# Optimization experiments

Measured on AMD Instinct MI355X. Metric: run time of the kernel, lower is better.

Reference implementation:

```python
import jax, jax.numpy as jnp
import numpy as np

NUM_ORDERS = 100
NUM_MACHINES = 40
NUM_AGVS = 64
EMBED = 128


def setup_inputs() -> dict:
    key = jax.random.key(0)
    ks = jax.random.split(key, 12)
    s = 0.05
    h_order = jax.random.normal(ks[0], (NUM_ORDERS, EMBED), jnp.float32)
    h_agv = jax.random.normal(ks[1], (NUM_AGVS, EMBED), jnp.float32)
    h_waiting = jax.random.normal(ks[2], (NUM_MACHINES, EMBED), jnp.float32)
    h_buffer = jax.random.normal(ks[3], (NUM_MACHINES, EMBED), jnp.float32)
    W1d = jax.random.normal(ks[4], (3 * EMBED, EMBED), jnp.float32) * s
    b1d = jnp.zeros((EMBED,), jnp.float32)
    W2d = jax.random.normal(ks[5], (EMBED,), jnp.float32) * s
    b2d = jnp.zeros((1,), jnp.float32)
    W1p = jax.random.normal(ks[6], (2 * EMBED, EMBED), jnp.float32) * s
    b1p = jnp.zeros((EMBED,), jnp.float32)
    W2p = jax.random.normal(ks[7], (EMBED,), jnp.float32) * s
    b2p = jnp.zeros((1,), jnp.float32)
    n_logits = NUM_AGVS * (NUM_ORDERS * NUM_MACHINES + NUM_MACHINES)
    action_mask = jax.random.randint(ks[8], (n_logits,), 0, 2).astype(jnp.int32)
    return dict(h_order=h_order, h_agv=h_agv, h_waiting=h_waiting, h_buffer=h_buffer,
                W1d=W1d, b1d=b1d, W2d=W2d, b2d=b2d,
                W1p=W1p, b1p=b1p, W2p=W2p, b2p=b2p,
                action_mask=action_mask)


def reference(h_order, h_agv, h_waiting, h_buffer,
              W1d, b1d, W2d, b2d, W1p, b1p, W2p, b2p, action_mask):
    O, M, A, D = NUM_ORDERS, NUM_MACHINES, NUM_AGVS, EMBED
    # dispatch pairs: order_idx = repeat_interleave(arange(O), M); machine_idx = tile(arange(M), O)
    order_idx = jnp.repeat(jnp.arange(O), M)            # [O*M]
    machine_idx = jnp.tile(jnp.arange(M), O)            # [O*M]
    pair = jnp.concatenate([h_order[order_idx], h_waiting[machine_idx]], axis=1)  # [O*M, 2D]
    agv_b = jnp.broadcast_to(h_agv[:, None, :], (A, O * M, D))                    # [A, O*M, D]
    disp_in = jnp.concatenate([agv_b, jnp.broadcast_to(pair[None], (A, O * M, 2 * D))], axis=-1)  # [A, O*M, 3D]
    hdd = jax.nn.relu(jnp.einsum('apf,fh->aph', disp_in, W1d) + b1d)
    disp_scores = jnp.einsum('aph,h->ap', hdd, W2d) + b2d[0]                      # [A, O*M]
    # pickup: concat(agv, buffer) per machine
    agv_p = jnp.broadcast_to(h_agv[:, None, :], (A, M, D))
    pick_in = jnp.concatenate([agv_p, jnp.broadcast_to(h_buffer[None], (A, M, D))], axis=-1)  # [A, M, 2D]
    hpp = jax.nn.relu(jnp.einsum('amf,fh->amh', pick_in, W1p) + b1p)
    pick_scores = jnp.einsum('amh,h->am', hpp, W2p) + b2p[0]                      # [A, M]
    logits = jnp.concatenate([disp_scores, pick_scores], axis=1).reshape(-1)      # [A*(O*M+M)]
    logits = jnp.where(action_mask == 0, -jnp.inf, logits)
    return logits
```

## Files before the change

### kernel.cpp

```cpp
#include <hip/hip_runtime.h>
#include <hip/hip_fp16.h>

#define NO 100
#define NM 40
#define NA 64
#define ND 128
#define PITCH 132

#define MASK_SENTINEL_BITS 0xFBFFu

typedef __half f16_t;
__device__ __forceinline__ float h2f(f16_t h) { return __half2float(h); }


__global__ __launch_bounds__(ND) void proj_kernel(
    const f16_t* __restrict__ h_order,
    const f16_t* __restrict__ h_agv,
    const f16_t* __restrict__ h_waiting,
    const f16_t* __restrict__ h_buffer,
    const f16_t* __restrict__ W1d,
    const f16_t* __restrict__ b1d,
    const f16_t* __restrict__ W1p,
    const f16_t* __restrict__ b1p,
    float* __restrict__ ws) {
  const int row = blockIdx.x;
  const int col = threadIdx.x;

  const f16_t* in;
  const f16_t* W;
  const f16_t* bias = nullptr;
  float* out;

  if (row < NA) {
    in = h_agv + row * ND;            W = W1d;                bias = b1d;
    out = ws + row * ND;
  } else if (row < NA + NO) {
    int r = row - NA;
    in = h_order + r * ND;            W = W1d + ND * ND;
    out = ws + (NA + r) * ND;
  } else if (row < NA + NO + NM) {
    int r = row - NA - NO;
    in = h_waiting + r * ND;          W = W1d + 2 * ND * ND;
    out = ws + (NA + NO + r) * ND;
  } else if (row < NA + NO + NM + NA) {
    int r = row - NA - NO - NM;
    in = h_agv + r * ND;              W = W1p;                bias = b1p;
    out = ws + (NA + NO + NM + r) * ND;
  } else {
    int r = row - NA - NO - NM - NA;
    in = h_buffer + r * ND;           W = W1p + ND * ND;
    out = ws + (NA + NO + NM + NA + r) * ND;
  }

  __shared__ float sIn[ND];
  sIn[col] = h2f(in[col]);
  __syncthreads();

  float acc = bias ? h2f(bias[col]) : 0.0f;
#pragma unroll 8
  for (int f = 0; f < ND; ++f) {
    acc += sIn[f] * h2f(W[f * ND + col]);
  }
  out[col] = acc;
}

__global__ __launch_bounds__(256) void score_kernel(
    const float* __restrict__ ws,
    const f16_t* __restrict__ W2d,
    const f16_t* __restrict__ b2d,
    const f16_t* __restrict__ W2p,
    const f16_t* __restrict__ b2p,
    const int* __restrict__ mask,
    unsigned short* __restrict__ out) {
  __shared__ float lds[25 * PITCH + 40 * PITCH + ND];
  const int tid = threadIdx.x;
  const int bid = blockIdx.x;
  const int per_agv = NO * NM + NM;

  if (bid < 256) {
    const int a = bid >> 2;
    const int o0 = (bid & 3) * 25;
    float* spo = lds;
    float* spw = lds + 25 * PITCH;
    float* sw2 = lds + 25 * PITCH + 40 * PITCH;

    const float4* paRow = (const float4*)(ws + a * ND);
    const float4* poBase = (const float4*)(ws + (NA + o0) * ND);
    for (int idx = tid; idx < 25 * (ND / 4); idx += 256) {
      int o = idx >> 5, c = idx & 31;
      float4 va = paRow[c], vo = poBase[o * (ND / 4) + c];
      float4 s = make_float4(va.x + vo.x, va.y + vo.y, va.z + vo.z, va.w + vo.w);
      *(float4*)(spo + o * PITCH + 4 * c) = s;
    }
    const float4* pwBase = (const float4*)(ws + (NA + NO) * ND);
    for (int idx = tid; idx < 40 * (ND / 4); idx += 256) {
      int m = idx >> 5, c = idx & 31;
      *(float4*)(spw + m * PITCH + 4 * c) = pwBase[m * (ND / 4) + c];
    }
    if (tid < ND) sw2[tid] = h2f(W2d[tid]);
    __syncthreads();

    if (tid >= 250) return;
    const int o = tid / 10;
    const int mb = tid % 10;
    const float* po_ = spo + o * PITCH;
    const float* pw_ = spw + mb * PITCH;

    float acc0 = 0.f, acc1 = 0.f, acc2 = 0.f, acc3 = 0.f;
#pragma unroll 4
    for (int i = 0; i < ND / 4; ++i) {
      float4 vo = *(const float4*)(po_ + 4 * i);
      float4 w0 = *(const float4*)(pw_ + 4 * i);
      float4 w1 = *(const float4*)(pw_ + 10 * PITCH + 4 * i);
      float4 w2v = *(const float4*)(pw_ + 20 * PITCH + 4 * i);
      float4 w3 = *(const float4*)(pw_ + 30 * PITCH + 4 * i);
      float4 ww = *(const float4*)(sw2 + 4 * i);
      acc0 += fmaxf(vo.x + w0.x, 0.f) * ww.x + fmaxf(vo.y + w0.y, 0.f) * ww.y +
              fmaxf(vo.z + w0.z, 0.f) * ww.z + fmaxf(vo.w + w0.w, 0.f) * ww.w;
      acc1 += fmaxf(vo.x + w1.x, 0.f) * ww.x + fmaxf(vo.y + w1.y, 0.f) * ww.y +
              fmaxf(vo.z + w1.z, 0.f) * ww.z + fmaxf(vo.w + w1.w, 0.f) * ww.w;
      acc2 += fmaxf(vo.x + w2v.x, 0.f) * ww.x + fmaxf(vo.y + w2v.y, 0.f) * ww.y +
              fmaxf(vo.z + w2v.z, 0.f) * ww.z + fmaxf(vo.w + w2v.w, 0.f) * ww.w;
      acc3 += fmaxf(vo.x + w3.x, 0.f) * ww.x + fmaxf(vo.y + w3.y, 0.f) * ww.y +
              fmaxf(vo.z + w3.z, 0.f) * ww.z + fmaxf(vo.w + w3.w, 0.f) * ww.w;
    }
    const float bd = h2f(b2d[0]);
    const int nbase = a * per_agv + (o0 + o) * NM + mb;
    float accs[4] = {acc0, acc1, acc2, acc3};
#pragma unroll
    for (int j = 0; j < 4; ++j) {
      int n = nbase + 10 * j;
      float val = fminf(fmaxf(accs[j] + bd, -60000.0f), 60000.0f);
      __half hv = __float2half(val);
      out[n] = (mask[n] == 0) ? (unsigned short)MASK_SENTINEL_BITS
                              : *(unsigned short*)&hv;
    }
  } else {
    const int a0 = (bid - 256) * 8;
    float* spa = lds;
    float* spb = lds + 8 * PITCH;
    float* sw2 = lds + 48 * PITCH;

    const float4* paBase = (const float4*)(ws + (NA + NO + NM) * ND);
    const float4* pbBase = (const float4*)(ws + (NA + NO + NM + NA) * ND);
    for (int idx = tid; idx < 8 * (ND / 4); idx += 256) {
      int r = idx >> 5, c = idx & 31;
      *(float4*)(spa + r * PITCH + 4 * c) = paBase[(a0 + r) * (ND / 4) + c];
    }
    for (int idx = tid; idx < 40 * (ND / 4); idx += 256) {
      int m = idx >> 5, c = idx & 31;
      *(float4*)(spb + m * PITCH + 4 * c) = pbBase[m * (ND / 4) + c];
    }
    if (tid < ND) sw2[tid] = h2f(W2p[tid]);
    __syncthreads();

    if (tid >= 320) return;
    const int a = a0 + tid / NM;
    const int m = tid % NM;
    const float* pa_ = spa + (tid / NM) * PITCH;
    const float* pb_ = spb + m * PITCH;
    float acc = 0.f;
#pragma unroll 4
    for (int i = 0; i < ND / 4; ++i) {
      float4 va = *(const float4*)(pa_ + 4 * i);
      float4 vb = *(const float4*)(pb_ + 4 * i);
      float4 ww = *(const float4*)(sw2 + 4 * i);
      acc += fmaxf(va.x + vb.x, 0.f) * ww.x + fmaxf(va.y + vb.y, 0.f) * ww.y +
             fmaxf(va.z + vb.z, 0.f) * ww.z + fmaxf(va.w + vb.w, 0.f) * ww.w;
    }
    float val = fminf(fmaxf(acc + h2f(b2p[0]), -60000.0f), 60000.0f);
    int n = a * per_agv + NO * NM + m;
    __half hv = __float2half(val);
    out[n] = (mask[n] == 0) ? (unsigned short)MASK_SENTINEL_BITS
                            : *(unsigned short*)&hv;
  }
}

extern "C" void kernel_launch(void* const* d_in, const int* in_sizes, int n_in,
                              void* d_out, int out_size, void* d_ws, size_t ws_size,
                              hipStream_t stream) {
  const f16_t* h_order   = (const f16_t*)d_in[0];
  const f16_t* h_agv     = (const f16_t*)d_in[1];
  const f16_t* h_waiting = (const f16_t*)d_in[2];
  const f16_t* h_buffer  = (const f16_t*)d_in[3];
  const f16_t* W1d       = (const f16_t*)d_in[4];
  const f16_t* b1d       = (const f16_t*)d_in[5];
  const f16_t* W2d       = (const f16_t*)d_in[6];
  const f16_t* b2d       = (const f16_t*)d_in[7];
  const f16_t* W1p       = (const f16_t*)d_in[8];
  const f16_t* b1p       = (const f16_t*)d_in[9];
  const f16_t* W2p       = (const f16_t*)d_in[10];
  const f16_t* b2p       = (const f16_t*)d_in[11];
  const int*   mask      = (const int*)d_in[12];
  unsigned short* out = (unsigned short*)d_out;
  float* ws = (float*)d_ws;

  proj_kernel<<<308, ND, 0, stream>>>(h_order, h_agv, h_waiting, h_buffer,
                                      W1d, b1d, W1p, b1p, ws);

  score_kernel<<<264, 256, 0, stream>>>(ws, W2d, b2d, W2p, b2p, mask, out);
}
```

Measured before the change: 91.35 us.

## Split proj reduction across 4 thread groups and double score grid over machines

After: 88.42 us. -3.2%, faster.

```diff
diff --git a/kernel.cpp b/kernel.cpp
--- a/kernel.cpp
+++ b/kernel.cpp
@@ -13,7 +13,7 @@
 __device__ __forceinline__ float h2f(f16_t h) { return __half2float(h); }
 
 
-__global__ __launch_bounds__(ND) void proj_kernel(
+__global__ __launch_bounds__(512) void proj_kernel(
     const f16_t* __restrict__ h_order,
     const f16_t* __restrict__ h_agv,
     const f16_t* __restrict__ h_waiting,
@@ -24,7 +24,9 @@
     const f16_t* __restrict__ b1p,
     float* __restrict__ ws) {
   const int row = blockIdx.x;
-  const int col = threadIdx.x;
+  const int tid = threadIdx.x;
+  const int col = tid & 127;
+  const int q = tid >> 7;
 
   const f16_t* in;
   const f16_t* W;
@@ -53,15 +55,23 @@
   }
 
   __shared__ float sIn[ND];
-  sIn[col] = h2f(in[col]);
+  __shared__ float sPart[4 * ND];
+  if (tid < ND) sIn[tid] = h2f(in[tid]);
   __syncthreads();
 
-  float acc = bias ? h2f(bias[col]) : 0.0f;
+  float acc = 0.0f;
+  const f16_t* Wq = W + (q * 32) * ND + col;
 #pragma unroll 8
-  for (int f = 0; f < ND; ++f) {
-    acc += sIn[f] * h2f(W[f * ND + col]);
-  }
-  out[col] = acc;
+  for (int f = 0; f < 32; ++f) {
+    acc += sIn[q * 32 + f] * h2f(Wq[f * ND]);
+  }
+  sPart[q * ND + col] = acc;
+  __syncthreads();
+  if (tid < ND) {
+    float r = sPart[tid] + sPart[ND + tid] + sPart[2 * ND + tid] +
+              sPart[3 * ND + tid] + (bias ? h2f(bias[tid]) : 0.0f);
+    out[tid] = r;
+  }
 }
 
 __global__ __launch_bounds__(256) void score_kernel(
@@ -72,28 +82,29 @@
     const f16_t* __restrict__ b2p,
     const int* __restrict__ mask,
     unsigned short* __restrict__ out) {
-  __shared__ float lds[25 * PITCH + 40 * PITCH + ND];
+  __shared__ float lds[48 * PITCH + ND];
   const int tid = threadIdx.x;
   const int bid = blockIdx.x;
   const int per_agv = NO * NM + NM;
 
-  if (bid < 256) {
-    const int a = bid >> 2;
-    const int o0 = (bid & 3) * 25;
+  if (bid < 512) {
+    const int a = bid >> 3;
+    const int o0 = ((bid & 7) >> 1) * 25;
+    const int m0 = (bid & 1) * 20;
     float* spo = lds;
     float* spw = lds + 25 * PITCH;
-    float* sw2 = lds + 25 * PITCH + 40 * PITCH;
+    float* sw2 = lds + 45 * PITCH;
 
     const float4* paRow = (const float4*)(ws + a * ND);
     const float4* poBase = (const float4*)(ws + (NA + o0) * ND);
     for (int idx = tid; idx < 25 * (ND / 4); idx += 256) {
       int o = idx >> 5, c = idx & 31;
       float4 va = paRow[c], vo = poBase[o * (ND / 4) + c];
-      float4 s = make_float4(va.x + vo.x, va.y + vo.y, va.z + vo.z, va.w + vo.w);
-      *(float4*)(spo + o * PITCH + 4 * c) = s;
-    }
-    const float4* pwBase = (const float4*)(ws + (NA + NO) * ND);
-    for (int idx = tid; idx < 40 * (ND / 4); idx += 256) {
+      *(float4*)(spo + o * PITCH + 4 * c) =
+          make_float4(va.x + vo.x, va.y + vo.y, va.z + vo.z, va.w + vo.w);
+    }
+    const float4* pwBase = (const float4*)(ws + (NA + NO + m0) * ND);
+    for (int idx = tid; idx < 20 * (ND / 4); idx += 256) {
       int m = idx >> 5, c = idx & 31;
       *(float4*)(spw + m * PITCH + 4 * c) = pwBase[m * (ND / 4) + c];
     }
@@ -106,29 +117,23 @@
     const float* po_ = spo + o * PITCH;
     const float* pw_ = spw + mb * PITCH;
 
-    float acc0 = 0.f, acc1 = 0.f, acc2 = 0.f, acc3 = 0.f;
-#pragma unroll 4
+    float acc0 = 0.f, acc1 = 0.f;
+#pragma unroll 8
     for (int i = 0; i < ND / 4; ++i) {
       float4 vo = *(const float4*)(po_ + 4 * i);
       float4 w0 = *(const float4*)(pw_ + 4 * i);
       float4 w1 = *(const float4*)(pw_ + 10 * PITCH + 4 * i);
-      float4 w2v = *(const float4*)(pw_ + 20 * PITCH + 4 * i);
-      float4 w3 = *(const float4*)(pw_ + 30 * PITCH + 4 * i);
       float4 ww = *(const float4*)(sw2 + 4 * i);
       acc0 += fmaxf(vo.x + w0.x, 0.f) * ww.x + fmaxf(vo.y + w0.y, 0.f) * ww.y +
               fmaxf(vo.z + w0.z, 0.f) * ww.z + fmaxf(vo.w + w0.w, 0.f) * ww.w;
       acc1 += fmaxf(vo.x + w1.x, 0.f) * ww.x + fmaxf(vo.y + w1.y, 0.f) * ww.y +
               fmaxf(vo.z + w1.z, 0.f) * ww.z + fmaxf(vo.w + w1.w, 0.f) * ww.w;
-      acc2 += fmaxf(vo.x + w2v.x, 0.f) * ww.x + fmaxf(vo.y + w2v.y, 0.f) * ww.y +
-              fmaxf(vo.z + w2v.z, 0.f) * ww.z + fmaxf(vo.w + w2v.w, 0.f) * ww.w;
-      acc3 += fmaxf(vo.x + w3.x, 0.f) * ww.x + fmaxf(vo.y + w3.y, 0.f) * ww.y +
-              fmaxf(vo.z + w3.z, 0.f) * ww.z + fmaxf(vo.w + w3.w, 0.f) * ww.w;
     }
     const float bd = h2f(b2d[0]);
-    const int nbase = a * per_agv + (o0 + o) * NM + mb;
-    float accs[4] = {acc0, acc1, acc2, acc3};
+    const int nbase = a * per_agv + (o0 + o) * NM + m0 + mb;
+    float accs[2] = {acc0, acc1};
 #pragma unroll
-    for (int j = 0; j < 4; ++j) {
+    for (int j = 0; j < 2; ++j) {
       int n = nbase + 10 * j;
       float val = fminf(fmaxf(accs[j] + bd, -60000.0f), 60000.0f);
       __half hv = __float2half(val);
@@ -136,7 +141,7 @@
                               : *(unsigned short*)&hv;
     }
   } else {
-    const int a0 = (bid - 256) * 8;
+    const int a0 = (bid - 512) * 8;
     float* spa = lds;
     float* spb = lds + 8 * PITCH;
     float* sw2 = lds + 48 * PITCH;
@@ -154,25 +159,27 @@
     if (tid < ND) sw2[tid] = h2f(W2p[tid]);
     __syncthreads();
 
-    if (tid >= 320) return;
-    const int a = a0 + tid / NM;
-    const int m = tid % NM;
-    const float* pa_ = spa + (tid / NM) * PITCH;
-    const float* pb_ = spb + m * PITCH;
-    float acc = 0.f;
-#pragma unroll 4
-    for (int i = 0; i < ND / 4; ++i) {
-      float4 va = *(const float4*)(pa_ + 4 * i);
-      float4 vb = *(const float4*)(pb_ + 4 * i);
-      float4 ww = *(const float4*)(sw2 + 4 * i);
-      acc += fmaxf(va.x + vb.x, 0.f) * ww.x + fmaxf(va.y + vb.y, 0.f) * ww.y +
-             fmaxf(va.z + vb.z, 0.f) * ww.z + fmaxf(va.w + vb.w, 0.f) * ww.w;
-    }
-    float val = fminf(fmaxf(acc + h2f(b2p[0]), -60000.0f), 60000.0f);
-    int n = a * per_agv + NO * NM + m;
-    __half hv = __float2half(val);
-    out[n] = (mask[n] == 0) ? (unsigned short)MASK_SENTINEL_BITS
-                            : *(unsigned short*)&hv;
+    const float bp = h2f(b2p[0]);
+    for (int p = tid; p < 8 * NM; p += 256) {
+      const int a = a0 + p / NM;
+      const int m = p % NM;
+      const float* pa_ = spa + (p / NM) * PITCH;
+      const float* pb_ = spb + m * PITCH;
+      float acc = 0.f;
+#pragma unroll 8
+      for (int i = 0; i < ND / 4; ++i) {
+        float4 va = *(const float4*)(pa_ + 4 * i);
+        float4 vb = *(const float4*)(pb_ + 4 * i);
+        float4 ww = *(const float4*)(sw2 + 4 * i);
+        acc += fmaxf(va.x + vb.x, 0.f) * ww.x + fmaxf(va.y + vb.y, 0.f) * ww.y +
+               fmaxf(va.z + vb.z, 0.f) * ww.z + fmaxf(va.w + vb.w, 0.f) * ww.w;
+      }
+      float val = fminf(fmaxf(acc + bp, -60000.0f), 60000.0f);
+      int n = a * per_agv + NO * NM + m;
+      __half hv = __float2half(val);
+      out[n] = (mask[n] == 0) ? (unsigned short)MASK_SENTINEL_BITS
+                              : *(unsigned short*)&hv;
+    }
   }
 }
 
@@ -195,8 +202,8 @@
   unsigned short* out = (unsigned short*)d_out;
   float* ws = (float*)d_ws;
 
-  proj_kernel<<<308, ND, 0, stream>>>(h_order, h_agv, h_waiting, h_buffer,
-                                      W1d, b1d, W1p, b1p, ws);
-
-  score_kernel<<<264, 256, 0, stream>>>(ws, W2d, b2d, W2p, b2p, mask, out);
+  proj_kernel<<<308, 512, 0, stream>>>(h_order, h_agv, h_waiting, h_buffer,
+                                       W1d, b1d, W1p, b1p, ws);
+
+  score_kernel<<<520, 256, 0, stream>>>(ws, W2d, b2d, W2p, b2p, mask, out);
 }
```
